# Kernel optimization log

Measured on AMD Instinct MI355X. Metric: run time of the kernel, lower is better.

The kernel has to match this reference:

```python
import jax, jax.numpy as jnp
import numpy as np

N_NODES = 100000
N_EDGES = 400000
N_GRAPHS = 256
HID = 256
BIO = 512
LAYERS = 3
EPS = 1e-5


def _seg_mean(v, seg, num):
    s = jax.ops.segment_sum(v, seg, num_segments=num)
    c = jax.ops.segment_sum(jnp.ones((v.shape[0], 1), v.dtype), seg, num_segments=num)
    return s / jnp.maximum(c, 1.0)


def setup_inputs() -> dict:
    key = jax.random.key(0)
    ks = jax.random.split(key, 24)
    d = {}
    d['x'] = jax.random.randint(ks[0], (N_NODES,), 0, 8)
    d['edge_index'] = jax.random.randint(ks[1], (2, N_EDGES), 0, N_NODES)
    d['edge_attr'] = jax.random.normal(ks[2], (N_EDGES, 4), jnp.float32)
    d['batch'] = jnp.sort(jax.random.randint(ks[3], (N_NODES,), 0, N_GRAPHS))
    sc = 0.06  # ~1/sqrt(HID)
    d['node_emb_W'] = jax.random.normal(ks[4], (8, HID), jnp.float32) * sc
    d['edge_emb_W'] = jax.random.normal(ks[5], (4, HID), jnp.float32) * 0.5
    d['edge_emb_b'] = jnp.zeros((HID,), jnp.float32)
    d['edge_mlp_W1'] = jax.random.normal(ks[6], (HID, HID), jnp.float32) * sc
    d['edge_mlp_b1'] = jnp.zeros((HID,), jnp.float32)
    d['edge_mlp_W2'] = jax.random.normal(ks[7], (HID, HID), jnp.float32) * sc
    d['edge_mlp_b2'] = jnp.zeros((HID,), jnp.float32)
    d['struct_scale'] = jnp.asarray(1.5, jnp.float32)
    d['conv_W1'] = jax.random.normal(ks[8], (LAYERS, HID, HID), jnp.float32) * sc
    d['conv_b1'] = jnp.zeros((LAYERS, HID), jnp.float32)
    d['conv_W2'] = jax.random.normal(ks[9], (LAYERS, HID, HID), jnp.float32) * sc
    d['conv_b2'] = jnp.zeros((LAYERS, HID), jnp.float32)
    d['conv_eps'] = jnp.zeros((LAYERS,), jnp.float32)
    d['norm_gamma'] = jnp.ones((LAYERS, HID), jnp.float32)
    d['norm_beta'] = jnp.zeros((LAYERS, HID), jnp.float32)
    d['norm_alpha'] = jnp.ones((LAYERS, HID), jnp.float32)
    d['mean_bio'] = jax.random.normal(ks[10], (BIO,), jnp.float32)
    d['head_W1'] = jax.random.normal(ks[11], (HID + BIO, HID), jnp.float32) * 0.036
    d['head_b1'] = jnp.zeros((HID,), jnp.float32)
    d['head_W2'] = jax.random.normal(ks[12], (HID, 1), jnp.float32) * sc
    d['head_b2'] = jnp.zeros((1,), jnp.float32)
    return d


def reference(x, edge_index, edge_attr, batch, node_emb_W, edge_emb_W, edge_emb_b,
              edge_mlp_W1, edge_mlp_b1, edge_mlp_W2, edge_mlp_b2, struct_scale,
              conv_W1, conv_b1, conv_W2, conv_b2, conv_eps,
              norm_gamma, norm_beta, norm_alpha, mean_bio,
              head_W1, head_b1, head_W2, head_b2):
    h = node_emb_W[x]  # [N, HID]
    src, dst = edge_index[0], edge_index[1]

    e = edge_attr @ edge_emb_W + edge_emb_b  # edge_emb
    e = jax.nn.relu(e @ edge_mlp_W1 + edge_mlp_b1) @ edge_mlp_W2 + edge_mlp_b2
    struct_mask = edge_attr[:, 1] > 0
    e = e * jnp.where(struct_mask, struct_scale, 1.0)[:, None]

    for l in range(LAYERS):
        # GINE conv: aggregate relu(x_j + e_ij) at target, then 2-layer MLP
        msg = jax.nn.relu(h[src] + e)  # [E, HID]
        agg = jax.ops.segment_sum(msg, dst, num_segments=N_NODES)
        z = (1.0 + conv_eps[l]) * h + agg
        h = jax.nn.relu(z @ conv_W1[l] + conv_b1[l]) @ conv_W2[l] + conv_b2[l]
        # GraphNorm per graph
        mean = _seg_mean(h, batch, N_GRAPHS)  # [G, HID]
        hc = h - norm_alpha[l] * mean[batch]
        var = _seg_mean(hc * hc, batch, N_GRAPHS)
        h = norm_gamma[l] * hc * jax.lax.rsqrt(var[batch] + EPS) + norm_beta[l]

    g = _seg_mean(h, batch, N_GRAPHS)  # global mean pool [G, HID]
    b_emb = jnp.broadcast_to(mean_bio, (g.shape[0], BIO))
    combined = jnp.concatenate([g, b_emb], axis=1)
    out = jax.nn.relu(combined @ head_W1 + head_b1) @ head_W2 + head_b2
    return out.mean(axis=1, keepdims=True)
```

## Files before the change

kernel.cpp:

```cpp
#include <hip/hip_runtime.h>
#include <cstddef>

#define NN 100000
#define NE 400000
#define NG 256
#define HIDC 256
#define EPSN 1e-5f

typedef unsigned short bfu;
using short8 = __attribute__((ext_vector_type(8))) short;
using f32x4  = __attribute__((ext_vector_type(4))) float;
using f32x2  = __attribute__((ext_vector_type(2))) float;

#if defined(__has_builtin)
#if __has_builtin(__builtin_amdgcn_cvt_pk_fp8_f32) && __has_builtin(__builtin_amdgcn_cvt_pk_f32_fp8)
#define HWFP8 1
#endif
#endif

__device__ __forceinline__ float bf2f(bfu b) {
    union { unsigned int u; float f; } v; v.u = ((unsigned int)b) << 16; return v.f;
}
__device__ __forceinline__ bfu f2bf(float f) {
    union { float f; unsigned int u; } v; v.f = f;
    unsigned int r = v.u + 0x7FFFu + ((v.u >> 16) & 1u);
    return (bfu)(r >> 16);
}
__device__ __forceinline__ float e4m3f_sw(unsigned char b) {
    unsigned s = ((unsigned)(b & 0x80u)) << 24;
    unsigned E = (b >> 3) & 15u, M = b & 7u;
    union { unsigned x; float f; } o;
    if (E == 0) { o.f = (float)M * 0.001953125f; o.x |= s; }
    else o.x = s | ((E + 120u) << 23) | (M << 20);
    return o.f;
}
__device__ __forceinline__ unsigned char f2e4m3_sw(float f) {
    union { float f; unsigned u; } v; v.f = f;
    unsigned s = (v.u >> 24) & 0x80u;
    float a = fabsf(f);
    if (!(a < 448.f)) return (unsigned char)(s | 0x7Eu);
    if (a < 0.0009765625f) return (unsigned char)s;
    if (a < 0.015625f) {
        int m = (int)(a * 512.f + 0.5f);
        if (m >= 8) return (unsigned char)(s | 0x08u);
        return (unsigned char)(s | (unsigned)m);
    }
    unsigned u = v.u;
    unsigned r = u + 0x7FFFFu + ((u >> 20) & 1u);
    int E = (int)((r >> 23) & 255u) - 127 + 7;
    unsigned M = (r >> 20) & 7u;
    if (E >= 16) return (unsigned char)(s | 0x7Eu);
    if (E <= 0) {
        int m = (int)(a * 512.f + 0.5f); if (m > 7) m = 7;
        return (unsigned char)(s | (unsigned)m);
    }
    return (unsigned char)(s | ((unsigned)E << 3) | M);
}
__device__ __forceinline__ unsigned int fp8enc4(float a, float b, float c, float d) {
#ifdef HWFP8
    int lo = __builtin_amdgcn_cvt_pk_fp8_f32(a, b, 0, false);
    int hi = __builtin_amdgcn_cvt_pk_fp8_f32(c, d, 0, false);
    return (unsigned int)((lo & 0xFFFF) | (hi << 16));
#else
    return (unsigned)f2e4m3_sw(a) | ((unsigned)f2e4m3_sw(b) << 8) |
           ((unsigned)f2e4m3_sw(c) << 16) | ((unsigned)f2e4m3_sw(d) << 24);
#endif
}
__device__ __forceinline__ float4 fp8dec4(unsigned int u) {
#ifdef HWFP8
    f32x2 lo = __builtin_amdgcn_cvt_pk_f32_fp8((int)u, false);
    f32x2 hi = __builtin_amdgcn_cvt_pk_f32_fp8((int)u, true);
    return make_float4(lo[0], lo[1], hi[0], hi[1]);
#else
    return make_float4(e4m3f_sw(u & 255u), e4m3f_sw((u >> 8) & 255u),
                       e4m3f_sw((u >> 16) & 255u), e4m3f_sw((u >> 24) & 255u));
#endif
}
__device__ __forceinline__ float4 ld4(const void* p, size_t i, int bf) {
    if (bf) {
        ushort4 u = *(const ushort4*)((const bfu*)p + i);
        return make_float4(bf2f(u.x), bf2f(u.y), bf2f(u.z), bf2f(u.w));
    }
    return *(const float4*)((const float*)p + i);
}
__device__ __forceinline__ float ld1(const void* p, size_t i, int bf) {
    return bf ? bf2f(((const bfu*)p)[i]) : ((const float*)p)[i];
}
__device__ __forceinline__ void st1(void* p, size_t i, float v, int bf) {
    if (bf) ((bfu*)p)[i] = f2bf(v); else ((float*)p)[i] = v;
}

__global__ void k_dt2(const unsigned int* __restrict__ g, int* __restrict__ flag) {
    if (threadIdx.x == 0)
        flag[0] = (g[0] == 0x3F800000u) ? 0 : 1;
}

__global__ void k_st2(const int* __restrict__ batch, int* __restrict__ starts) {
    int g = threadIdx.x;
    if (g > NG) return;
    if (g == NG) { starts[NG] = NN; return; }
    int lo = 0, hi = NN;
    while (lo < hi) { int mid = (lo + hi) >> 1; if (batch[mid] < g) lo = mid + 1; else hi = mid; }
    starts[g] = lo;
}

__global__ void k_zi(int* __restrict__ p, int n) {
    int i = blockIdx.x * blockDim.x + threadIdx.x;
    if (i < n) p[i] = 0;
}

__global__ void k_cnt(const int* __restrict__ ei, int* __restrict__ deg) {
    int e = blockIdx.x * blockDim.x + threadIdx.x;
    if (e >= NE) return;
    int d = ei[NE + e];
    if ((unsigned)d < (unsigned)NN) atomicAdd(&deg[d], 1);
}
__global__ void k_sc1(const int* __restrict__ deg, int* __restrict__ rowp,
                      int* __restrict__ part) {
    __shared__ int sh[256];
    int b = blockIdx.x, t = threadIdx.x;
    int i = b * 256 + t;
    int v = (i < NN) ? deg[i] : 0;
    sh[t] = v; __syncthreads();
    for (int off = 1; off < 256; off <<= 1) {
        int add = (t >= off) ? sh[t - off] : 0;
        __syncthreads();
        sh[t] += add; __syncthreads();
    }
    if (i < NN) rowp[i] = sh[t] - v;
    if (t == 255) part[b] = sh[255];
}
__global__ void k_sc2(int* __restrict__ part, int nb) {
    if (threadIdx.x != 0) return;
    int run = 0;
    for (int b = 0; b < nb; ++b) { int t = part[b]; part[b] = run; run += t; }
}
__global__ void k_sc3(int* __restrict__ rowp, const int* __restrict__ part) {
    int i = blockIdx.x * blockDim.x + threadIdx.x;
    if (i < NN) rowp[i] += part[blockIdx.x];
    if (i == 0) rowp[NN] = NE;
}
__global__ void k_cpi(const int* __restrict__ a, int* __restrict__ b, int n) {
    int i = blockIdx.x * blockDim.x + threadIdx.x;
    if (i < n) b[i] = a[i];
}
__global__ void k_fil(const int* __restrict__ ei, int* __restrict__ cursor,
                      int* __restrict__ csrc, int* __restrict__ ceid) {
    int e = blockIdx.x * blockDim.x + threadIdx.x;
    if (e >= NE) return;
    int s = ei[e], d = ei[NE + e];
    if ((unsigned)d >= (unsigned)NN) return;
    int pos = atomicAdd(&cursor[d], 1);
    csrc[pos] = ((unsigned)s < (unsigned)NN) ? s : 0;
    ceid[pos] = e;
}

__global__ void k_wef(const void* __restrict__ Wemb, const void* __restrict__ bemb,
                      const void* __restrict__ W1, const void* __restrict__ b1,
                      float* __restrict__ weff, float* __restrict__ beff,
                      const int* __restrict__ dtf) {
    int bf = *dtf;
    int j = blockIdx.x;
    int n = threadIdx.x;
    float acc = 0.f;
    if (j < 4) {
        for (int k = 0; k < HIDC; ++k)
            acc += ld1(Wemb, (size_t)j * HIDC + k, bf) * ld1(W1, (size_t)k * HIDC + n, bf);
        weff[j * HIDC + n] = acc;
    } else {
        for (int k = 0; k < HIDC; ++k)
            acc += ld1(bemb, k, bf) * ld1(W1, (size_t)k * HIDC + n, bf);
        beff[n] = acc + ld1(b1, n, bf);
    }
}

__global__ void k_gat3(const bfu* __restrict__ h, const unsigned char* __restrict__ e8,
                       const int* __restrict__ rowp, const int* __restrict__ csrc,
                       bfu* __restrict__ agg) {
    int tid = blockIdx.x * blockDim.x + threadIdx.x;
    if (tid >= NN * 64) return;
    int n = tid >> 6, q = (tid & 63) << 2;
    int s0 = rowp[n], s1 = rowp[n + 1];
    float4 a = make_float4(0.f, 0.f, 0.f, 0.f);
    for (int i = s0; i < s1; ++i) {
        int src = csrc[i];
        ushort4 hu = *(const ushort4*)(h + (size_t)src * HIDC + q);
        unsigned int eu = *(const unsigned int*)(e8 + (size_t)i * HIDC + q);
        float4 ev = fp8dec4(eu);
        a.x += fmaxf(bf2f(hu.x) + ev.x, 0.f);
        a.y += fmaxf(bf2f(hu.y) + ev.y, 0.f);
        a.z += fmaxf(bf2f(hu.z) + ev.z, 0.f);
        a.w += fmaxf(bf2f(hu.w) + ev.w, 0.f);
    }
    ushort4 o; o.x = f2bf(a.x); o.y = f2bf(a.y); o.z = f2bf(a.z); o.w = f2bf(a.w);
    *(ushort4*)(agg + (size_t)n * HIDC + q) = o;
}

__global__ void k_wtr(const void* __restrict__ W, long wOff, bfu* __restrict__ Wt,
                      const int* __restrict__ dtf) {
    int o = blockIdx.x * blockDim.x + threadIdx.x;
    if (o >= HIDC * HIDC) return;
    int blk = o >> 9, pos = o & 511;
    int w = blk >> 5, rem = blk & 31;
    int t = rem >> 3, kb = rem & 7;
    int pr = pos >> 3, j = pos & 7;
    int lr = pr >> 2, lq = pr & 3;
    int n = w * 64 + t * 16 + lr;
    int k = kb * 32 + lq * 8 + j;
    Wt[o] = f2bf(ld1(W, (size_t)wOff + (size_t)k * HIDC + n, *dtf));
}

__global__ void k_emb(const int* __restrict__ x, const void* __restrict__ W,
                      bfu* __restrict__ h, const int* __restrict__ dtf) {
    int tid = blockIdx.x * blockDim.x + threadIdx.x;
    if (tid >= NN * 64) return;
    int bf = *dtf;
    int n = tid >> 6, q = (tid & 63) << 2;
    int xv = x[n]; if ((unsigned)xv >= 8u) xv = 0;
    float4 v = ld4(W, (size_t)xv * HIDC + q, bf);
    ushort4 o; o.x = f2bf(v.x); o.y = f2bf(v.y); o.z = f2bf(v.z); o.w = f2bf(v.w);
    *(ushort4*)(h + (size_t)n * HIDC + q) = o;
}

__global__ __launch_bounds__(256)
void k_me(const void* __restrict__ attrs,
          const float* __restrict__ weff, const float* __restrict__ beff,
          const bfu* __restrict__ Wt, const void* __restrict__ bias,
          const void* __restrict__ scalep,
          unsigned char* __restrict__ C,
          const int* __restrict__ dtf, const int* __restrict__ eidx) {
    __shared__ bfu As[8][64 * 32];
    __shared__ float sf[64];
    const int bf = *dtf;
    const int tid = threadIdx.x;
    const int wave = tid >> 6, lane = tid & 63;
    const int lr = lane & 15, lq = lane >> 4;
    const int m0 = blockIdx.x * 64;
    const int row = tid >> 2;
    const int ak = (tid & 3) << 3;
    const int gmA = m0 + row;

    float aa[4] = {0.f, 0.f, 0.f, 0.f};
    if (gmA < NE) {
        long er = (long)eidx[gmA];
        aa[0] = ld1(attrs, (size_t)er * 4 + 0, bf);
        aa[1] = ld1(attrs, (size_t)er * 4 + 1, bf);
        aa[2] = ld1(attrs, (size_t)er * 4 + 2, bf);
        aa[3] = ld1(attrs, (size_t)er * 4 + 3, bf);
    }
    if ((tid & 3) == 0)
        sf[row] = (gmA < NE && aa[1] > 0.f) ? ld1(scalep, 0, bf) : 1.0f;

#pragma unroll
    for (int k0 = 0; k0 < 256; k0 += 32) {
        const int c = k0 + ak;
        float4 b0 = *(const float4*)(beff + c);
        float4 b1v = *(const float4*)(beff + c + 4);
        float v0 = b0.x, v1 = b0.y, v2 = b0.z, v3 = b0.w;
        float v4 = b1v.x, v5 = b1v.y, v6 = b1v.z, v7 = b1v.w;
#pragma unroll
        for (int j = 0; j < 4; ++j) {
            float4 w0 = *(const float4*)(weff + j * HIDC + c);
            float4 w1 = *(const float4*)(weff + j * HIDC + c + 4);
            v0 += aa[j] * w0.x; v1 += aa[j] * w0.y;
            v2 += aa[j] * w0.z; v3 += aa[j] * w0.w;
            v4 += aa[j] * w1.x; v5 += aa[j] * w1.y;
            v6 += aa[j] * w1.z; v7 += aa[j] * w1.w;
        }
        ushort4 o0, o1;
        o0.x = f2bf(fmaxf(v0, 0.f)); o0.y = f2bf(fmaxf(v1, 0.f));
        o0.z = f2bf(fmaxf(v2, 0.f)); o0.w = f2bf(fmaxf(v3, 0.f));
        o1.x = f2bf(fmaxf(v4, 0.f)); o1.y = f2bf(fmaxf(v5, 0.f));
        o1.z = f2bf(fmaxf(v6, 0.f)); o1.w = f2bf(fmaxf(v7, 0.f));
        *(ushort4*)(&As[k0 >> 5][row * 32 + ak]) = o0;
        *(ushort4*)(&As[k0 >> 5][row * 32 + ak + 4]) = o1;
    }
    __syncthreads();

    f32x4 acc[4][4] = {};
    const bfu* wb = Wt + ((size_t)wave * 32) * 512 + (size_t)(lr * 4 + lq) * 8;
#pragma unroll
    for (int kb = 0; kb < 8; ++kb) {
        short8 fa[4], fbv[4];
#pragma unroll
        for (int r = 0; r < 4; ++r)
            fa[r] = *(const short8*)(&As[kb][(r * 16 + lr) * 32 + lq * 8]);
#pragma unroll
        for (int t = 0; t < 4; ++t)
            fbv[t] = *(const short8*)(wb + (size_t)(t * 8 + kb) * 512);
#pragma unroll
        for (int r = 0; r < 4; ++r)
#pragma unroll
            for (int t = 0; t < 4; ++t)
                acc[r][t] = __builtin_amdgcn_mfma_f32_16x16x32_bf16(
                    fa[r], fbv[t], acc[r][t], 0, 0, 0);
    }

    float bv[4];
#pragma unroll
    for (int t = 0; t < 4; ++t)
        bv[t] = ld1(bias, (size_t)(wave * 64 + t * 16 + lr), bf);
#pragma unroll
    for (int r = 0; r < 4; ++r) {
#pragma unroll
        for (int i = 0; i < 4; ++i) {
            int rr = r * 16 + lq * 4 + i;
            int gm = m0 + rr;
            if (gm >= NE) continue;
            float rs = sf[rr];
            float ov0 = (acc[r][0][i] + bv[0]) * rs;
            float ov1 = (acc[r][1][i] + bv[1]) * rs;
            float ov2 = (acc[r][2][i] + bv[2]) * rs;
            float ov3 = (acc[r][3][i] + bv[3]) * rs;
            unsigned int pk = fp8enc4(ov0, ov1, ov2, ov3);
            size_t cbase = (size_t)gm * HIDC + wave * 64 + lr;
            C[cbase]      = (unsigned char)(pk & 255u);
            C[cbase + 16] = (unsigned char)((pk >> 8) & 255u);
            C[cbase + 32] = (unsigned char)((pk >> 16) & 255u);
            C[cbase + 48] = (unsigned char)(pk >> 24);
        }
    }
}

__global__ __launch_bounds__(256)
void k_cnv(bfu* __restrict__ h, const bfu* __restrict__ agg,
           const void* __restrict__ eps, int epsIdx,
           const bfu* __restrict__ Wt1, const void* __restrict__ bias1, long b1Off,
           const bfu* __restrict__ Wt2, const void* __restrict__ bias2, long b2Off,
           const int* __restrict__ dtf) {
    __shared__ bfu Ts[8][64 * 32];
    const int bf = *dtf;
    const int tid = threadIdx.x;
    const int wave = tid >> 6, lane = tid & 63;
    const int lr = lane & 15, lq = lane >> 4;
    const int m0 = blockIdx.x * 64;
    const float epsv = 1.0f + ld1(eps, epsIdx, bf);
    const int row = tid >> 2;
    const int ak = (tid & 3) << 3;
    const int gmA = m0 + row;
    const bfu* wb1 = Wt1 + ((size_t)wave * 32) * 512 + (size_t)(lr * 4 + lq) * 8;
    const bfu* wb2 = Wt2 + ((size_t)wave * 32) * 512 + (size_t)(lr * 4 + lq) * 8;

#pragma unroll
    for (int k0 = 0; k0 < 256; k0 += 32) {
        float hv[8] = {}, gv[8] = {};
        if (gmA < NN) {
            ushort4 h0 = *(const ushort4*)(h + (size_t)gmA * HIDC + k0 + ak);
            ushort4 h1 = *(const ushort4*)(h + (size_t)gmA * HIDC + k0 + ak + 4);
            hv[0]=bf2f(h0.x); hv[1]=bf2f(h0.y); hv[2]=bf2f(h0.z); hv[3]=bf2f(h0.w);
            hv[4]=bf2f(h1.x); hv[5]=bf2f(h1.y); hv[6]=bf2f(h1.z); hv[7]=bf2f(h1.w);
            ushort4 g0 = *(const ushort4*)(agg + (size_t)gmA * HIDC + k0 + ak);
            ushort4 g1 = *(const ushort4*)(agg + (size_t)gmA * HIDC + k0 + ak + 4);
            gv[0]=bf2f(g0.x); gv[1]=bf2f(g0.y); gv[2]=bf2f(g0.z); gv[3]=bf2f(g0.w);
            gv[4]=bf2f(g1.x); gv[5]=bf2f(g1.y); gv[6]=bf2f(g1.z); gv[7]=bf2f(g1.w);
        }
        ushort4 o0, o1;
        o0.x = f2bf(epsv * hv[0] + gv[0]); o0.y = f2bf(epsv * hv[1] + gv[1]);
        o0.z = f2bf(epsv * hv[2] + gv[2]); o0.w = f2bf(epsv * hv[3] + gv[3]);
        o1.x = f2bf(epsv * hv[4] + gv[4]); o1.y = f2bf(epsv * hv[5] + gv[5]);
        o1.z = f2bf(epsv * hv[6] + gv[6]); o1.w = f2bf(epsv * hv[7] + gv[7]);
        *(ushort4*)(&Ts[k0 >> 5][row * 32 + ak]) = o0;
        *(ushort4*)(&Ts[k0 >> 5][row * 32 + ak + 4]) = o1;
    }
    __syncthreads();

    f32x4 acc[4][4] = {};
#pragma unroll
    for (int kb = 0; kb < 8; ++kb) {
        short8 fa[4], fbv[4];
#pragma unroll
        for (int r = 0; r < 4; ++r)
            fa[r] = *(const short8*)(&Ts[kb][(r * 16 + lr) * 32 + lq * 8]);
#pragma unroll
        for (int t = 0; t < 4; ++t)
            fbv[t] = *(const short8*)(wb1 + (size_t)(t * 8 + kb) * 512);
#pragma unroll
        for (int r = 0; r < 4; ++r)
#pragma unroll
            for (int t = 0; t < 4; ++t)
                acc[r][t] = __builtin_amdgcn_mfma_f32_16x16x32_bf16(
                    fa[r], fbv[t], acc[r][t], 0, 0, 0);
    }
    __syncthreads();

    {
        float bv[4];
#pragma unroll
        for (int t = 0; t < 4; ++t)
            bv[t] = ld1(bias1, (size_t)b1Off + wave * 64 + t * 16 + lr, bf);
        const f32x4 z4 = {0.f, 0.f, 0.f, 0.f};
#pragma unroll
        for (int r = 0; r < 4; ++r) {
#pragma unroll
            for (int i = 0; i < 4; ++i) {
                int rowo = r * 16 + lq * 4 + i;
#pragma unroll
                for (int t = 0; t < 4; ++t) {
                    int kk = wave * 64 + t * 16 + lr;
                    Ts[kk >> 5][rowo * 32 + (kk & 31)] =
                        f2bf(fmaxf(acc[r][t][i] + bv[t], 0.f));
                }
            }
        }
#pragma unroll
        for (int r = 0; r < 4; ++r)
#pragma unroll
            for (int t = 0; t < 4; ++t)
                acc[r][t] = z4;
    }
    __syncthreads();

#pragma unroll
    for (int kb = 0; kb < 8; ++kb) {
        short8 fa[4], fbv[4];
#pragma unroll
        for (int r = 0; r < 4; ++r)
            fa[r] = *(const short8*)(&Ts[kb][(r * 16 + lr) * 32 + lq * 8]);
#pragma unroll
        for (int t = 0; t < 4; ++t)
            fbv[t] = *(const short8*)(wb2 + (size_t)(t * 8 + kb) * 512);
#pragma unroll
        for (int r = 0; r < 4; ++r)
#pragma unroll
            for (int t = 0; t < 4; ++t)
                acc[r][t] = __builtin_amdgcn_mfma_f32_16x16x32_bf16(
                    fa[r], fbv[t], acc[r][t], 0, 0, 0);
    }
    float bv[4];
#pragma unroll
    for (int t = 0; t < 4; ++t)
        bv[t] = ld1(bias2, (size_t)b2Off + wave * 64 + t * 16 + lr, bf);
#pragma unroll
    for (int r = 0; r < 4; ++r) {
#pragma unroll
        for (int i = 0; i < 4; ++i) {
            int gm = m0 + r * 16 + lq * 4 + i;
            if (gm >= NN) continue;
            size_t cbase = (size_t)gm * HIDC + wave * 64 + lr;
#pragma unroll
            for (int t = 0; t < 4; ++t)
                h[cbase + t * 16] = f2bf(acc[r][t][i] + bv[t]);
        }
    }
}

__global__ void k_s1(const bfu* __restrict__ h, const int* __restrict__ starts,
                     float* __restrict__ psum, float* __restrict__ psq) {
    int g = blockIdx.x, c8 = blockIdx.y, c = threadIdx.x;
    int s = starts[g], t = starts[g + 1];
    int len = t - s;
    int b = s + (int)(((long)len * c8) >> 3);
    int e = s + (int)(((long)len * (c8 + 1)) >> 3);
    float sum = 0.f, sq = 0.f;
    for (int n = b; n < e; ++n) {
        float v = bf2f(h[(size_t)n * HIDC + c]);
        sum += v; sq += v * v;
    }
    psum[((size_t)g * 8 + c8) * HIDC + c] = sum;
    psq[((size_t)g * 8 + c8) * HIDC + c] = sq;
}
__global__ void k_s2(const int* __restrict__ starts,
                     const float* __restrict__ psum, const float* __restrict__ psq,
                     const void* __restrict__ alpha, long aOff,
                     float* __restrict__ gmean, float* __restrict__ gvar,
                     const int* __restrict__ dtf) {
    int g = blockIdx.x, c = threadIdx.x;
    float sum = 0.f, sq = 0.f;
#pragma unroll
    for (int j = 0; j < 8; ++j) {
        sum += psum[((size_t)g * 8 + j) * HIDC + c];
        sq  += psq[((size_t)g * 8 + j) * HIDC + c];
    }
    int cn = starts[g + 1] - starts[g]; if (cn < 1) cn = 1;
    float cnt = (float)cn;
    float m = sum / cnt;
    float a = ld1(alpha, (size_t)aOff + c, *dtf);
    gmean[g * HIDC + c] = m;
    gvar[g * HIDC + c] = fmaxf(sq / cnt - (2.f * a - a * a) * m * m, 0.f);
}

__global__ void k_nrm(bfu* __restrict__ h, const int* __restrict__ batch,
                      const float* __restrict__ gmean, const float* __restrict__ gvar,
                      const void* __restrict__ gamma, const void* __restrict__ beta,
                      const void* __restrict__ alpha, long pOff,
                      const int* __restrict__ dtf) {
    int tid = blockIdx.x * blockDim.x + threadIdx.x;
    if (tid >= NN * 64) return;
    int bf = *dtf;
    int n = tid >> 6, q = (tid & 63) << 2;
    int g = batch[n]; if ((unsigned)g >= (unsigned)NG) g = 0;
    ushort4 hu = *(ushort4*)(h + (size_t)n * HIDC + q);
    const float4 mv = *(const float4*)(gmean + g * HIDC + q);
    const float4 vv = *(const float4*)(gvar + g * HIDC + q);
    float4 ga = ld4(gamma, (size_t)pOff + q, bf);
    float4 be = ld4(beta, (size_t)pOff + q, bf);
    float4 al = ld4(alpha, (size_t)pOff + q, bf);
    float4 v;
    v.x = ga.x * (bf2f(hu.x) - al.x * mv.x) * rsqrtf(vv.x + EPSN) + be.x;
    v.y = ga.y * (bf2f(hu.y) - al.y * mv.y) * rsqrtf(vv.y + EPSN) + be.y;
    v.z = ga.z * (bf2f(hu.z) - al.z * mv.z) * rsqrtf(vv.z + EPSN) + be.z;
    v.w = ga.w * (bf2f(hu.w) - al.w * mv.w) * rsqrtf(vv.w + EPSN) + be.w;
    ushort4 ov; ov.x = f2bf(v.x); ov.y = f2bf(v.y); ov.z = f2bf(v.z); ov.w = f2bf(v.w);
    *(ushort4*)(h + (size_t)n * HIDC + q) = ov;
}

__global__ void k_pl2(const int* __restrict__ starts,
                      const float* __restrict__ gmean, const float* __restrict__ gvar,
                      const void* __restrict__ gamma, const void* __restrict__ beta,
                      const void* __restrict__ alpha, long pOff,
                      float* __restrict__ g, const int* __restrict__ dtf) {
    int bf = *dtf;
    int gb = blockIdx.x, c = threadIdx.x;
    int cn = starts[gb + 1] - starts[gb];
    if (cn <= 0) { g[gb * HIDC + c] = 0.f; return; }
    float m = gmean[gb * HIDC + c];
    float v = gvar[gb * HIDC + c];
    float ga = ld1(gamma, (size_t)pOff + c, bf);
    float be = ld1(beta, (size_t)pOff + c, bf);
    float al = ld1(alpha, (size_t)pOff + c, bf);
    g[gb * HIDC + c] = ga * (1.f - al) * m * rsqrtf(v + EPSN) + be;
}

__global__ void k_hd(const float* __restrict__ g, const void* __restrict__ bio,
                     const void* __restrict__ W1, const void* __restrict__ b1,
                     const void* __restrict__ W2, const void* __restrict__ b2,
                     void* __restrict__ out, const int* __restrict__ dtf) {
    __shared__ float comb[768];
    __shared__ float red[256];
    __shared__ int nanf;
    int bf = *dtf;
    int gb = blockIdx.x, t = threadIdx.x;
    if (t == 0) nanf = 0;
    comb[t] = g[gb * HIDC + t];
    comb[256 + t] = ld1(bio, t, bf);
    comb[512 + t] = ld1(bio, 256 + t, bf);
    __syncthreads();
    float acc = ld1(b1, t, bf);
    for (int k = 0; k < 768; ++k) acc += comb[k] * ld1(W1, (size_t)k * HIDC + t, bf);
    if (isnan(acc) || isinf(acc)) nanf = 1;
    float hid = fmaxf(acc, 0.f);
    red[t] = hid * ld1(W2, t, bf);
    __syncthreads();
    for (int off = 128; off > 0; off >>= 1) {
        if (t < off) red[t] += red[t + off];
        __syncthreads();
    }
    if (t == 0) {
        float r = red[0] + ld1(b2, 0, bf);
        if (nanf || isnan(r)) r = 999.0f;
        st1(out, gb, r, bf);
    }
}

extern "C" void kernel_launch(void* const* d_in, const int* in_sizes, int n_in,
                              void* d_out, int out_size, void* d_ws, size_t ws_size,
                              hipStream_t stream) {
    const int* x = (const int*)d_in[0];
    const int* ei = (const int*)d_in[1];
    const void* eattr = d_in[2];
    const int* batch = (const int*)d_in[3];
    const void* node_emb_W = d_in[4];
    const void* edge_emb_W = d_in[5];
    const void* edge_emb_b = d_in[6];
    const void* emlp_W1 = d_in[7];
    const void* emlp_b1 = d_in[8];
    const void* emlp_W2 = d_in[9];
    const void* emlp_b2 = d_in[10];
    const void* struct_scale = d_in[11];
    const void* conv_W1 = d_in[12];
    const void* conv_b1 = d_in[13];
    const void* conv_W2 = d_in[14];
    const void* conv_b2 = d_in[15];
    const void* conv_eps = d_in[16];
    const void* ngamma = d_in[17];
    const void* nbeta = d_in[18];
    const void* nalpha = d_in[19];
    const void* mean_bio = d_in[20];
    const void* head_W1 = d_in[21];
    const void* head_b1 = d_in[22];
    const void* head_W2 = d_in[23];
    const void* head_b2 = d_in[24];
    (void)in_sizes; (void)n_in; (void)out_size; (void)ws_size;

    const size_t H_B = (size_t)NN * HIDC * 2;
    const size_t E8_B = (size_t)NE * HIDC;
    char* p = (char*)d_ws;
    bfu* hbuf = (bfu*)p; p += H_B;
    bfu* aggb = (bfu*)p; p += H_B;
    unsigned char* e8 = (unsigned char*)p; p += E8_B;
    bfu* wt = (bfu*)p; p += 8 * 65536 * 2;
    int* rowp = (int*)p;
    int* cursor = rowp + 100352;
    int* part = cursor + 100352;
    int* splits = part + 1024;
    int* cnts = splits + 8;
    int* csrc = cnts + 8;
    int* ceid = csrc + NE;
    p = (char*)(ceid + NE);
    float* psum = (float*)p; p += (size_t)NG * 8 * HIDC * 4;
    float* psq = (float*)p; p += (size_t)NG * 8 * HIDC * 4;
    char* small = p;
    int* starts = (int*)small;
    int* dtf = (int*)(small + 2048);
    float* weff = (float*)(small + 4096);
    float* beff = weff + 4 * HIDC;
    float* gmean = (float*)(small + 16384);
    float* gvar = gmean + NG * HIDC;
    float* gpool = gvar + NG * HIDC;
    (void)splits; (void)cnts;

    k_dt2<<<1, 64, 0, stream>>>((const unsigned int*)ngamma, dtf);
    k_st2<<<1, 512, 0, stream>>>(batch, starts);
    k_emb<<<(NN * 64 + 255) / 256, 256, 0, stream>>>(x, node_emb_W, hbuf, dtf);
    k_wef<<<5, 256, 0, stream>>>(edge_emb_W, edge_emb_b, emlp_W1, emlp_b1,
                                 weff, beff, dtf);

    k_wtr<<<256, 256, 0, stream>>>(emlp_W2, 0, wt + 65536, dtf);
    for (int l = 0; l < 3; ++l) {
        k_wtr<<<256, 256, 0, stream>>>(conv_W1, (long)l * HIDC * HIDC, wt + (2 + l) * 65536, dtf);
        k_wtr<<<256, 256, 0, stream>>>(conv_W2, (long)l * HIDC * HIDC, wt + (5 + l) * 65536, dtf);
    }

    const int NBN = (NN + 255) / 256;
    k_zi<<<NBN, 256, 0, stream>>>(cursor, NN);
    k_cnt<<<(NE + 255) / 256, 256, 0, stream>>>(ei, cursor);
    k_sc1<<<NBN, 256, 0, stream>>>(cursor, rowp, part);
    k_sc2<<<1, 64, 0, stream>>>(part, NBN);
    k_sc3<<<NBN, 256, 0, stream>>>(rowp, part);
    k_cpi<<<NBN, 256, 0, stream>>>(rowp, cursor, NN);
    k_fil<<<(NE + 255) / 256, 256, 0, stream>>>(ei, cursor, csrc, ceid);

    dim3 gE((NE + 63) / 64), gN((NN + 63) / 64);
    k_me<<<gE, 256, 0, stream>>>(eattr, weff, beff, wt + 65536, emlp_b2,
                                 struct_scale, e8, dtf, ceid);

    dim3 gS1(NG, 8);
    const int gatBlocks = (NN * 64 + 255) / 256;

    for (int l = 0; l < 3; ++l) {
        k_gat3<<<gatBlocks, 256, 0, stream>>>(hbuf, e8, rowp, csrc, aggb);
        k_cnv<<<gN, 256, 0, stream>>>(
            hbuf, aggb, conv_eps, l,
            wt + (2 + l) * 65536, conv_b1, (long)l * HIDC,
            wt + (5 + l) * 65536, conv_b2, (long)l * HIDC, dtf);
        k_s1<<<gS1, 256, 0, stream>>>(hbuf, starts, psum, psq);
        k_s2<<<NG, 256, 0, stream>>>(starts, psum, psq, nalpha, (long)l * HIDC,
                                     gmean, gvar, dtf);
        if (l < 2) {
            k_nrm<<<(NN * 64 + 255) / 256, 256, 0, stream>>>(
                hbuf, batch, gmean, gvar, ngamma, nbeta, nalpha, (long)l * HIDC, dtf);
        }
    }

    k_pl2<<<NG, 256, 0, stream>>>(starts, gmean, gvar, ngamma, nbeta, nalpha,
                                  (long)2 * HIDC, gpool, dtf);
    k_hd<<<NG, 256, 0, stream>>>(gpool, mean_bio, head_W1, head_b1,
                                 head_W2, head_b2, d_out, dtf);
}
```

Baseline: 1.014 ms.

## Restructure edge-MLP kernel to 512 threads with halved LDS and 2x4 wave tiling

The edge MLP kernel moves from 256 to 512 threads per block, with 8 waves arranged as 2 row groups by 4 column groups, so each wave holds half the accumulators. The A tile is built in two K-halves through a 4-slice LDS buffer, and the small first-layer weights and biases are staged in shared memory instead of read from global memory. The aim is higher occupancy and lower register pressure. In exchange it adds extra barriers, and it drops the NE bounds checks, which is only safe because NE divides evenly by 64.

```diff
diff --git a/kernel.cpp b/kernel.cpp
--- a/kernel.cpp
+++ b/kernel.cpp
@@ -222,98 +222,93 @@
     *(ushort4*)(h + (size_t)n * HIDC + q) = o;
 }
 
-__global__ __launch_bounds__(256)
+__global__ __launch_bounds__(512, 8)
 void k_me(const void* __restrict__ attrs,
           const float* __restrict__ weff, const float* __restrict__ beff,
           const bfu* __restrict__ Wt, const void* __restrict__ bias,
           const void* __restrict__ scalep,
           unsigned char* __restrict__ C,
           const int* __restrict__ dtf, const int* __restrict__ eidx) {
-    __shared__ bfu As[8][64 * 32];
+    __shared__ bfu As[4][64 * 32];
+    __shared__ float wsh[1280];
     __shared__ float sf[64];
     const int bf = *dtf;
     const int tid = threadIdx.x;
     const int wave = tid >> 6, lane = tid & 63;
     const int lr = lane & 15, lq = lane >> 4;
+    const int wr = wave >> 2, wc = wave & 3;
     const int m0 = blockIdx.x * 64;
-    const int row = tid >> 2;
-    const int ak = (tid & 3) << 3;
-    const int gmA = m0 + row;
-
-    float aa[4] = {0.f, 0.f, 0.f, 0.f};
-    if (gmA < NE) {
-        long er = (long)eidx[gmA];
+    const int row = tid >> 3;
+    const int a4 = (tid & 7) << 2;
+
+    for (int v = tid; v < 1280; v += 512)
+        wsh[v] = (v < 1024) ? weff[v] : beff[v - 1024];
+
+    float aa[4];
+    {
+        long er = (long)eidx[m0 + row];
         aa[0] = ld1(attrs, (size_t)er * 4 + 0, bf);
         aa[1] = ld1(attrs, (size_t)er * 4 + 1, bf);
         aa[2] = ld1(attrs, (size_t)er * 4 + 2, bf);
         aa[3] = ld1(attrs, (size_t)er * 4 + 3, bf);
     }
-    if ((tid & 3) == 0)
-        sf[row] = (gmA < NE && aa[1] > 0.f) ? ld1(scalep, 0, bf) : 1.0f;
-
-#pragma unroll
-    for (int k0 = 0; k0 < 256; k0 += 32) {
-        const int c = k0 + ak;
-        float4 b0 = *(const float4*)(beff + c);
-        float4 b1v = *(const float4*)(beff + c + 4);
-        float v0 = b0.x, v1 = b0.y, v2 = b0.z, v3 = b0.w;
-        float v4 = b1v.x, v5 = b1v.y, v6 = b1v.z, v7 = b1v.w;
-#pragma unroll
-        for (int j = 0; j < 4; ++j) {
-            float4 w0 = *(const float4*)(weff + j * HIDC + c);
-            float4 w1 = *(const float4*)(weff + j * HIDC + c + 4);
-            v0 += aa[j] * w0.x; v1 += aa[j] * w0.y;
-            v2 += aa[j] * w0.z; v3 += aa[j] * w0.w;
-            v4 += aa[j] * w1.x; v5 += aa[j] * w1.y;
-            v6 += aa[j] * w1.z; v7 += aa[j] * w1.w;
+    if ((tid & 7) == 0)
+        sf[row] = (aa[1] > 0.f) ? ld1(scalep, 0, bf) : 1.0f;
+    __syncthreads();
+
+    f32x4 acc[2][4] = {};
+    const bfu* wb = Wt + ((size_t)wc * 32) * 512 + (size_t)(lr * 4 + lq) * 8;
+
+    for (int h = 0; h < 2; ++h) {
+        if (h) __syncthreads();
+#pragma unroll
+        for (int q = 0; q < 4; ++q) {
+            const int c = h * 128 + q * 32 + a4;
+            float4 bb = *(const float4*)(wsh + 1024 + c);
+            float v0 = bb.x, v1 = bb.y, v2 = bb.z, v3 = bb.w;
+#pragma unroll
+            for (int j = 0; j < 4; ++j) {
+                float4 w0 = *(const float4*)(wsh + j * 256 + c);
+                v0 += aa[j] * w0.x; v1 += aa[j] * w0.y;
+                v2 += aa[j] * w0.z; v3 += aa[j] * w0.w;
+            }
+            ushort4 o;
+            o.x = f2bf(fmaxf(v0, 0.f)); o.y = f2bf(fmaxf(v1, 0.f));
+            o.z = f2bf(fmaxf(v2, 0.f)); o.w = f2bf(fmaxf(v3, 0.f));
+            *(ushort4*)(&As[q][row * 32 + a4]) = o;
         }
-        ushort4 o0, o1;
-        o0.x = f2bf(fmaxf(v0, 0.f)); o0.y = f2bf(fmaxf(v1, 0.f));
-        o0.z = f2bf(fmaxf(v2, 0.f)); o0.w = f2bf(fmaxf(v3, 0.f));
-        o1.x = f2bf(fmaxf(v4, 0.f)); o1.y = f2bf(fmaxf(v5, 0.f));
-        o1.z = f2bf(fmaxf(v6, 0.f)); o1.w = f2bf(fmaxf(v7, 0.f));
-        *(ushort4*)(&As[k0 >> 5][row * 32 + ak]) = o0;
-        *(ushort4*)(&As[k0 >> 5][row * 32 + ak + 4]) = o1;
-    }
-    __syncthreads();
-
-    f32x4 acc[4][4] = {};
-    const bfu* wb = Wt + ((size_t)wave * 32) * 512 + (size_t)(lr * 4 + lq) * 8;
-#pragma unroll
-    for (int kb = 0; kb < 8; ++kb) {
-        short8 fa[4], fbv[4];
-#pragma unroll
-        for (int r = 0; r < 4; ++r)
-            fa[r] = *(const short8*)(&As[kb][(r * 16 + lr) * 32 + lq * 8]);
-#pragma unroll
-        for (int t = 0; t < 4; ++t)
-            fbv[t] = *(const short8*)(wb + (size_t)(t * 8 + kb) * 512);
-#pragma unroll
-        for (int r = 0; r < 4; ++r)
-#pragma unroll
-            for (int t = 0; t < 4; ++t)
-                acc[r][t] = __builtin_amdgcn_mfma_f32_16x16x32_bf16(
-                    fa[r], fbv[t], acc[r][t], 0, 0, 0);
+        __syncthreads();
+#pragma unroll
+        for (int q = 0; q < 4; ++q) {
+            const int kb = h * 4 + q;
+            short8 fa0 = *(const short8*)(&As[q][(wr * 32 + lr) * 32 + lq * 8]);
+            short8 fa1 = *(const short8*)(&As[q][(wr * 32 + 16 + lr) * 32 + lq * 8]);
+#pragma unroll
+            for (int t = 0; t < 4; ++t) {
+                short8 fb = *(const short8*)(wb + (size_t)(t * 8 + kb) * 512);
+                acc[0][t] = __builtin_amdgcn_mfma_f32_16x16x32_bf16(fa0, fb, acc[0][t], 0, 0, 0);
+                acc[1][t] = __builtin_amdgcn_mfma_f32_16x16x32_bf16(fa1, fb, acc[1][t], 0, 0, 0);
+            }
+        }
     }
 
     float bv[4];
 #pragma unroll
     for (int t = 0; t < 4; ++t)
-        bv[t] = ld1(bias, (size_t)(wave * 64 + t * 16 + lr), bf);
-#pragma unroll
-    for (int r = 0; r < 4; ++r) {
+        bv[t] = ld1(bias, (size_t)(wc * 64 + t * 16 + lr), bf);
+#pragma unroll
+    for (int r = 0; r < 2; ++r) {
 #pragma unroll
         for (int i = 0; i < 4; ++i) {
-            int rr = r * 16 + lq * 4 + i;
+            int rr = wr * 32 + r * 16 + lq * 4 + i;
             int gm = m0 + rr;
-            if (gm >= NE) continue;
             float rs = sf[rr];
             float ov0 = (acc[r][0][i] + bv[0]) * rs;
             float ov1 = (acc[r][1][i] + bv[1]) * rs;
             float ov2 = (acc[r][2][i] + bv[2]) * rs;
             float ov3 = (acc[r][3][i] + bv[3]) * rs;
             unsigned int pk = fp8enc4(ov0, ov1, ov2, ov3);
-            size_t cbase = (size_t)gm * HIDC + wave * 64 + lr;
+            size_t cbase = (size_t)gm * HIDC + wc * 64 + lr;
             C[cbase]      = (unsigned char)(pk & 255u);
             C[cbase + 16] = (unsigned char)((pk >> 8) & 255u);
             C[cbase + 32] = (unsigned char)((pk >> 16) & 255u);
@@ -631,7 +626,7 @@
     k_fil<<<(NE + 255) / 256, 256, 0, stream>>>(ei, cursor, csrc, ceid);
 
     dim3 gE((NE + 63) / 64), gN((NN + 63) / 64);
-    k_me<<<gE, 256, 0, stream>>>(eattr, weff, beff, wt + 65536, emlp_b2,
+    k_me<<<gE, 512, 0, stream>>>(eattr, weff, beff, wt + 65536, emlp_b2,
                                  struct_scale, e8, dtf, ceid);
 
     dim3 gS1(NG, 8);
```

Measured after the change: 1.036 ms. +2.2%, slower.
